# Kernel tuning notes

Hardware: AMD Instinct MI355X
Metric: run time of the kernel (lower is better)

The kernel has to match this reference:

```python
import jax, jax.numpy as jnp
import numpy as np


def _conv(x, w, b, pad):
    # x: [N,C,H,W], w: [O,C,kh,kw]
    out = jax.lax.conv_general_dilated(
        x, w, window_strides=(1, 1), padding=[(pad, pad), (pad, pad)],
        dimension_numbers=("NCHW", "OIHW", "NCHW"))
    return out + b[None, :, None, None]


def _deform_conv(x, offset, mask, w, b):
    # Modulated deformable conv (DCNv2), 3x3 kernel, stride 1, pad 1, dilation 1.
    # x: [N,C,H,W], offset: [N,18,H,W] (per-point (dy,dx) pairs), mask: [N,9,H,W]
    N, C, H, W = x.shape
    KK = 9
    off = offset.reshape(N, KK, 2, H, W)
    dy, dx = off[:, :, 0], off[:, :, 1]            # [N,9,H,W]
    k = jnp.arange(3, dtype=x.dtype) - 1.0         # kernel taps -1,0,1
    ky = jnp.repeat(k, 3)                          # row-major 3x3 order
    kx = jnp.tile(k, 3)
    py = dy + ky[None, :, None, None] + jnp.arange(H, dtype=x.dtype)[None, None, :, None]
    px = dx + kx[None, :, None, None] + jnp.arange(W, dtype=x.dtype)[None, None, None, :]
    y0 = jnp.floor(py)
    x0 = jnp.floor(px)
    wy = (py - y0)[..., None]                      # [N,9,H,W,1]
    wx = (px - x0)[..., None]
    x_t = x.transpose(0, 2, 3, 1).reshape(N, H * W, C)  # [N,HW,C]

    def gather(iy, ix):
        valid = ((iy >= 0) & (iy < H) & (ix >= 0) & (ix < W)).astype(x.dtype)
        idx = (jnp.clip(iy, 0, H - 1).astype(jnp.int32) * W
               + jnp.clip(ix, 0, W - 1).astype(jnp.int32)).reshape(N, -1)
        v = jax.vmap(lambda a, i: a[i])(x_t, idx).reshape(N, KK, H, W, C)
        return v * valid[..., None]

    v00 = gather(y0, x0)
    v01 = gather(y0, x0 + 1)
    v10 = gather(y0 + 1, x0)
    v11 = gather(y0 + 1, x0 + 1)
    samp = (v00 * (1 - wy) * (1 - wx) + v01 * (1 - wy) * wx
            + v10 * wy * (1 - wx) + v11 * wy * wx)
    samp = samp * mask[..., None]                  # modulation
    O = w.shape[0]
    out = jnp.einsum("nkhwc,ock->nohw", samp, w.reshape(O, C, KK))
    return out + b[None, :, None, None]


def _res_block(x, w1, b1, w2, b2):
    # ResidualBlock_noBN: x + conv2(relu(conv1(x)))
    return x + _conv(jax.nn.relu(_conv(x, w1, b1, 1)), w2, b2, 1)


def setup_inputs() -> dict:
    key = jax.random.key(0)
    ks = jax.random.split(key, 16)
    f = jnp.float32

    def rn(k, shape, scale):
        return jax.random.normal(k, shape, dtype=f) * scale

    N, C, H, W = 2, 64, 128, 128
    inp = {}
    inp["xd"] = rn(ks[0], (N, 2 * C, H // 2, W // 2), 1.0)
    inp["xl"] = rn(ks[1], (N, C, H, W), 1.0)
    inp["xr"] = rn(ks[2], (N, C, H, W), 1.0)
    inp["up_w"] = rn(ks[3], (C, 2 * C, 2, 2), (2 * C * 4) ** -0.5)
    inp["up_b"] = jnp.zeros((C,), f)
    inp["offl_w"] = rn(ks[4], (27, 3 * C, 3, 3), 0.01 * (3 * C * 9) ** -0.5)
    inp["offl_b"] = jnp.zeros((27,), f)
    inp["dl_w"] = rn(ks[5], (C, C, 3, 3), (C * 9) ** -0.5)
    inp["dl_b"] = jnp.zeros((C,), f)
    inp["offr_w"] = rn(ks[6], (27, 3 * C, 3, 3), 0.01 * (3 * C * 9) ** -0.5)
    inp["offr_b"] = jnp.zeros((27,), f)
    inp["dr_w"] = rn(ks[7], (C, C, 3, 3), (C * 9) ** -0.5)
    inp["dr_b"] = jnp.zeros((C,), f)
    inp["cv_w"] = rn(ks[8], (C, 3 * C, 3, 3), (3 * C * 9) ** -0.5)
    inp["cv_b"] = jnp.zeros((C,), f)
    for i, nm in enumerate(["rb1_w1", "rb1_w2", "rb2_w1", "rb2_w2"]):
        inp[nm] = rn(ks[9 + i], (C, C, 3, 3), (C * 9) ** -0.5)
    for nm in ["rb1_b1", "rb1_b2", "rb2_b1", "rb2_b2"]:
        inp[nm] = jnp.zeros((C,), f)
    return inp


def reference(xd, xl, xr, up_w, up_b, offl_w, offl_b, dl_w, dl_b,
              offr_w, offr_b, dr_w, dr_b, cv_w, cv_b,
              rb1_w1, rb1_b1, rb1_w2, rb1_b2,
              rb2_w1, rb2_b1, rb2_w2, rb2_b2):
    # UP_SAMPLE: nearest x2 upsample, then k=2 conv (pad 0 -> size 2H-1)
    xd = jnp.repeat(jnp.repeat(xd, 2, axis=2), 2, axis=3)
    xd = _conv(xd, up_w, up_b, 0)
    dY = xl.shape[2] - xd.shape[2]
    dX = xl.shape[3] - xd.shape[3]
    xd = jnp.pad(xd, ((0, 0), (0, 0), (dY // 2, dY - dY // 2), (dX // 2, dX - dX // 2)))
    # left deform branch
    ol = _conv(jnp.concatenate([xl, xr, xd], axis=1), offl_w, offl_b, 1)
    off_l = ol[:, :18]                    # cat(o1, o2)
    mask_l = jax.nn.sigmoid(ol[:, 18:])
    xl = _deform_conv(xl, off_l, mask_l, dl_w, dl_b)
    # right deform branch (uses updated xl)
    orr = _conv(jnp.concatenate([xl, xr, xd], axis=1), offr_w, offr_b, 1)
    off_r = orr[:, :18]
    mask_r = jax.nn.sigmoid(orr[:, 18:])
    xr = _deform_conv(xr, off_r, mask_r, dr_w, dr_b)
    # CONV_BLOCK: conv+relu then two residual blocks
    x = jnp.concatenate([xl, xr, xd], axis=1)
    x = jax.nn.relu(_conv(x, cv_w, cv_b, 1))
    x = _res_block(x, rb1_w1, rb1_b1, rb1_w2, rb1_b2)
    x = _res_block(x, rb2_w1, rb2_b1, rb2_w2, rb2_b2)
    return x
```

## Files before the change

kernel.cpp:

```cpp
#include <hip/hip_runtime.h>
#include <math.h>

#define HW 16384

typedef unsigned short u16;
typedef __attribute__((ext_vector_type(8))) short short8;
typedef __attribute__((ext_vector_type(16))) float f32x16;

union U16B {
  uint4 u;
  short8 v;
  u16 s[8];
};

__device__ inline u16 f2b(float f) {
  unsigned u = __float_as_uint(f);
  u += 0x7FFF + ((u >> 16) & 1);
  return (u16)(u >> 16);
}
__device__ inline float b2f(u16 h) {
  return __uint_as_float(((unsigned)h) << 16);
}

__device__ inline u16 pack_frag(const float* __restrict__ w, int Cin, int O,
                                int OT, int d) {
  int j = d & 7;
  int lane = (d >> 3) & 63;
  int rest = d >> 9;
  int ot = rest % OT; rest /= OT;
  int ks = rest & 3; rest >>= 2;
  int kx = rest % 3; rest /= 3;
  int ky = rest % 3; int s = rest / 3;
  int och = ot * 32 + (lane & 31);
  int ch = s * 64 + ks * 16 + ((lane >> 5) << 3) + j;
  if (och >= O) return 0;
  return f2b(w[((size_t)och * Cin + ch) * 9 + ky * 3 + kx]);
}

__device__ inline u16 pack_def(const float* __restrict__ w, int d) {
  int j = d & 7;
  int lane = (d >> 3) & 63;
  int g = d >> 9;
  int ot = g & 1;
  int t = g >> 1;
  int ks = t & 3;
  int k = t >> 2;
  int och = ot * 32 + (lane & 31);
  int c = ks * 16 + ((lane >> 5) << 3) + j;
  return f2b(w[((size_t)och * 64 + c) * 9 + k]);
}

__device__ inline u16 pack_up(const float* __restrict__ w, int d) {
  int j = d & 7;
  int lane = (d >> 3) & 63;
  int g = d >> 9;
  int ot = g & 1;
  int rest = g >> 1;
  int ks = rest & 7;
  int t = rest >> 3;
  int och = ot * 32 + (lane & 31);
  int ci = ks * 16 + ((lane >> 5) << 3) + j;
  return f2b(w[((size_t)och * 128 + ci) * 4 + t]);
}

__global__ __launch_bounds__(256) void setup_kernel(
    const float* __restrict__ dl_w, const float* __restrict__ dr_w,
    const float* __restrict__ up_w, const float* __restrict__ cv_w,
    const float* __restrict__ offl_w, const float* __restrict__ offr_w,
    const float* __restrict__ r1a, const float* __restrict__ r1b,
    const float* __restrict__ r2a, const float* __restrict__ r2b,
    u16* __restrict__ wup, u16* __restrict__ wdl, u16* __restrict__ wdr,
    u16* __restrict__ wcv, u16* __restrict__ wofl, u16* __restrict__ wofr,
    u16* __restrict__ wr1a, u16* __restrict__ wr1b,
    u16* __restrict__ wr2a, u16* __restrict__ wr2b,
    const float* __restrict__ xl, const float* __restrict__ xr,
    u16* __restrict__ xlh, u16* __restrict__ xrh,
    const float* __restrict__ xd, u16* __restrict__ xdh) {
  __shared__ float sT[8448];
  int tid = threadIdx.x;
  int b = blockIdx.x;
  if (b < 1856) {
    int d = b * 256 + tid;
    if (d < 32768) { wup[d] = pack_up(up_w, d); return; }
    d -= 32768;
    if (d < 36864) { wdl[d] = pack_def(dl_w, d); return; }
    d -= 36864;
    if (d < 36864) { wdr[d] = pack_def(dr_w, d); return; }
    d -= 36864;
    if (d < 110592) { wcv[d] = pack_frag(cv_w, 192, 64, 2, d); return; }
    d -= 110592;
    if (d < 55296) { wofl[d] = pack_frag(offl_w, 192, 27, 1, d); return; }
    d -= 55296;
    if (d < 55296) { wofr[d] = pack_frag(offr_w, 192, 27, 1, d); return; }
    d -= 55296;
    if (d < 36864) { wr1a[d] = pack_frag(r1a, 64, 64, 2, d); return; }
    d -= 36864;
    if (d < 36864) { wr1b[d] = pack_frag(r1b, 64, 64, 2, d); return; }
    d -= 36864;
    if (d < 36864) { wr2a[d] = pack_frag(r2a, 64, 64, 2, d); return; }
    d -= 36864;
    if (d < 36864) { wr2b[d] = pack_frag(r2b, 64, 64, 2, d); return; }
    return;
  }
  b -= 1856;
  if (b < 512) {
    int y = b & 127;
    int pid = b >> 7;
    const float* src = (pid >> 1) ? xr : xl;
    u16* dst = (pid >> 1) ? xrh : xlh;
    int n = pid & 1;
#pragma unroll
    for (int i = 0; i < 8; ++i) {
      int q = tid + i * 256;
      int ch = q >> 5, pxq = q & 31;
      float4 v = *(const float4*)(src + ((size_t)(n * 64 + ch)) * HW + y * 128 + pxq * 4);
      *(float4*)&sT[ch * 132 + pxq * 4] = v;
    }
    __syncthreads();
    int px = tid >> 1, half = tid & 1;
    u16* op = dst + (((size_t)(n * 128 + y)) * 128 + px) * 64 + half * 32;
#pragma unroll
    for (int c = 0; c < 4; ++c) {
      uint4 v;
      int ob = (half * 32 + c * 8);
      v.x = (unsigned)f2b(sT[(ob + 0) * 132 + px]) | ((unsigned)f2b(sT[(ob + 1) * 132 + px]) << 16);
      v.y = (unsigned)f2b(sT[(ob + 2) * 132 + px]) | ((unsigned)f2b(sT[(ob + 3) * 132 + px]) << 16);
      v.z = (unsigned)f2b(sT[(ob + 4) * 132 + px]) | ((unsigned)f2b(sT[(ob + 5) * 132 + px]) << 16);
      v.w = (unsigned)f2b(sT[(ob + 6) * 132 + px]) | ((unsigned)f2b(sT[(ob + 7) * 132 + px]) << 16);
      *(uint4*)(op + c * 8) = v;
    }
    return;
  }
  b -= 512;
  {
    int r = b & 63;
    int n = b >> 6;
#pragma unroll
    for (int i = 0; i < 8; ++i) {
      int q = tid + i * 256;
      int ch = q >> 4, col4 = q & 15;
      float4 v = *(const float4*)(xd + ((size_t)(n * 128 + ch) * 64 + r) * 64 + col4 * 4);
      *(float4*)&sT[ch * 66 + col4 * 4] = v;
    }
    __syncthreads();
#pragma unroll
    for (int i = 0; i < 4; ++i) {
      int q = tid + i * 256;
      int col = q >> 4, cho = q & 15;
      uint4 v;
      int cb = cho * 8;
      v.x = (unsigned)f2b(sT[(cb + 0) * 66 + col]) | ((unsigned)f2b(sT[(cb + 1) * 66 + col]) << 16);
      v.y = (unsigned)f2b(sT[(cb + 2) * 66 + col]) | ((unsigned)f2b(sT[(cb + 3) * 66 + col]) << 16);
      v.z = (unsigned)f2b(sT[(cb + 4) * 66 + col]) | ((unsigned)f2b(sT[(cb + 5) * 66 + col]) << 16);
      v.w = (unsigned)f2b(sT[(cb + 6) * 66 + col]) | ((unsigned)f2b(sT[(cb + 7) * 66 + col]) << 16);
      *(uint4*)(xdh + (((size_t)(n * 64 + r)) * 64 + col) * 128 + cb) = v;
    }
  }
}

__global__ __launch_bounds__(1024) void upconv_mf(
    const u16* __restrict__ xdh, const u16* __restrict__ wup,
    const float* __restrict__ bias, u16* __restrict__ outH) {
  __shared__ float s_red[4][3][16][64];
  const int tid = threadIdx.x;
  const int lane = tid & 63;
  const int w = tid >> 6;
  const int p2 = w >> 2;
  const int t = w & 3;
  const int y = blockIdx.x;
  const int n = blockIdx.y;
  const int px = (p2 << 5) + (lane & 31);
  const int h = lane >> 5;

  f32x16 acc0, acc1;
#pragma unroll
  for (int i = 0; i < 16; ++i) { acc0[i] = 0.f; acc1[i] = 0.f; }

  const u16* xb = xdh + ((size_t)n * 64 * 64) * 128;
  const int ty = t >> 1, tx = t & 1;
  const int row = min((y + ty) >> 1, 63);
  const int col = min((px + tx) >> 1, 63);
  const u16* src = xb + ((size_t)(row * 64 + col)) * 128;
#pragma unroll
  for (int ks = 0; ks < 8; ++ks) {
    U16B bf;
    bf.u = *(const uint4*)(src + ks * 16 + h * 8);
    const u16* wp = wup + ((size_t)((t * 8 + ks) * 2)) * 512 + lane * 8;
    U16B a0, a1;
    a0.u = *(const uint4*)wp;
    a1.u = *(const uint4*)(wp + 512);
    acc0 = __builtin_amdgcn_mfma_f32_32x32x16_bf16(a0.v, bf.v, acc0, 0, 0, 0);
    acc1 = __builtin_amdgcn_mfma_f32_32x32x16_bf16(a1.v, bf.v, acc1, 0, 0, 0);
  }

  const bool zero = (y == 127) || (px == 127);
  const size_t pixb = (((size_t)(n * 128 + y)) * 128 + px) * 64;

  if (t != 0) {
#pragma unroll
    for (int i = 0; i < 16; ++i) s_red[p2][t - 1][i][lane] = acc0[i];
  }
  __syncthreads();
  if (t == 0) {
#pragma unroll
    for (int q = 0; q < 4; ++q) {
      int oo = 8 * q + 4 * h;
      float v[4];
#pragma unroll
      for (int r = 0; r < 4; ++r) {
        int i = q * 4 + r;
        float s = acc0[i] + s_red[p2][0][i][lane] + s_red[p2][1][i][lane] +
                  s_red[p2][2][i][lane];
        v[r] = zero ? 0.f : (s + bias[oo + r]);
      }
      ushort4 hh;
      hh.x = f2b(v[0]); hh.y = f2b(v[1]); hh.z = f2b(v[2]); hh.w = f2b(v[3]);
      *(ushort4*)(outH + pixb + oo) = hh;
    }
  }
  __syncthreads();
  if (t != 0) {
#pragma unroll
    for (int i = 0; i < 16; ++i) s_red[p2][t - 1][i][lane] = acc1[i];
  }
  __syncthreads();
  if (t == 0) {
#pragma unroll
    for (int q = 0; q < 4; ++q) {
      int oo = 32 + 8 * q + 4 * h;
      float v[4];
#pragma unroll
      for (int r = 0; r < 4; ++r) {
        int i = q * 4 + r;
        float s = acc1[i] + s_red[p2][0][i][lane] + s_red[p2][1][i][lane] +
                  s_red[p2][2][i][lane];
        v[r] = zero ? 0.f : (s + bias[oo + r]);
      }
      ushort4 hh;
      hh.x = f2b(v[0]); hh.y = f2b(v[1]); hh.z = f2b(v[2]); hh.w = f2b(v[3]);
      *(ushort4*)(outH + pixb + oo) = hh;
    }
  }
}

template <int NSEG>
__global__ __launch_bounds__(1024) void mfconv_s(
    const u16* __restrict__ in0, const u16* __restrict__ in1,
    const u16* __restrict__ in2, const u16* __restrict__ wpk,
    const float* __restrict__ bias, const u16* __restrict__ resh,
    float* __restrict__ outF, u16* __restrict__ outH, int mode) {
  __shared__ __align__(16) unsigned char s_un[49920];
  u16* stg = (u16*)s_un;
  float* s_redf = (float*)s_un;

  const int tid = threadIdx.x;
  const int lane = tid & 63;
  const int w = tid >> 6;
  const int p2 = w >> 2;
  const int kq = w & 3;
  const int y = blockIdx.x;
  const int n = blockIdx.y;
  const int px = (p2 << 5) + (lane & 31);
  const int h = lane >> 5;
  const int gpx = lane >> 3;
  const int gcs = lane & 7;

  auto stg_at = [&](int e, int cg, int p) -> u16* {
    return stg + (((e * 8 + cg) * 130 + p) << 3);
  };

  f32x16 acc0, acc1;
#pragma unroll
  for (int i = 0; i < 16; ++i) { acc0[i] = 0.f; acc1[i] = 0.f; }

  for (int s = 0; s < NSEG; ++s) {
    const u16* sp = (s == 0) ? in0 : ((s == 1) ? in1 : in2);
    const u16* bn = sp + ((size_t)n * 128) * 128 * 64;
    for (int i = w; i < 48; i += 16) {
      int ky = i >> 4, g = i & 15;
      int row = y + ky - 1;
      int ppx = g * 8 + gpx;
      uint4 v = make_uint4(0, 0, 0, 0);
      if ((unsigned)row < 128u)
        v = *(const uint4*)(bn + (size_t)row * (128 * 64) + (size_t)ppx * 64 + gcs * 8);
      *(uint4*)stg_at(ky, gcs, ppx) = v;
    }
    __syncthreads();
#pragma unroll
    for (int ky = 0; ky < 3; ++ky) {
#pragma unroll
      for (int kx = 0; kx < 3; ++kx) {
        int pxc = px + kx - 1;
        bool valid = (unsigned)pxc < 128u;
        int pxcc = min(max(pxc, 0), 127);
        U16B bf;
        bf.u = *(const uint4*)stg_at(ky, kq * 2 + h, pxcc);
        if (!valid) bf.u = make_uint4(0, 0, 0, 0);
        const u16* wp = wpk +
            ((size_t)((((s * 3 + ky) * 3 + kx) * 4 + kq) * 2)) * 512 + lane * 8;
        U16B a0, a1;
        a0.u = *(const uint4*)wp;
        a1.u = *(const uint4*)(wp + 512);
        acc0 = __builtin_amdgcn_mfma_f32_32x32x16_bf16(a0.v, bf.v, acc0, 0, 0, 0);
        acc1 = __builtin_amdgcn_mfma_f32_32x32x16_bf16(a1.v, bf.v, acc1, 0, 0, 0);
      }
    }
    __syncthreads();
  }

  const size_t pixb = ((size_t)(n * 128 + y)) * 128 + px;

  if (kq != 0) {
#pragma unroll
    for (int i = 0; i < 16; ++i)
      s_redf[((p2 * 3 + (kq - 1)) * 16 + i) * 64 + lane] = acc0[i];
  }
  __syncthreads();
  if (kq == 0) {
#pragma unroll
    for (int q = 0; q < 4; ++q) {
      int oo = 8 * q + 4 * h;
      float v[4];
#pragma unroll
      for (int r = 0; r < 4; ++r) {
        int i = q * 4 + r;
        v[r] = acc0[i] + s_redf[((p2 * 3 + 0) * 16 + i) * 64 + lane] +
               s_redf[((p2 * 3 + 1) * 16 + i) * 64 + lane] +
               s_redf[((p2 * 3 + 2) * 16 + i) * 64 + lane] + bias[oo + r];
      }
      if (mode == 1) {
#pragma unroll
        for (int r = 0; r < 4; ++r) v[r] = fmaxf(v[r], 0.f);
      } else if (mode == 3) {
        ushort4 rv = *(const ushort4*)(resh + pixb * 64 + oo);
        v[0] += b2f(rv.x); v[1] += b2f(rv.y); v[2] += b2f(rv.z); v[3] += b2f(rv.w);
      }
      if (outH) {
        ushort4 hh;
        hh.x = f2b(v[0]); hh.y = f2b(v[1]); hh.z = f2b(v[2]); hh.w = f2b(v[3]);
        *(ushort4*)(outH + pixb * 64 + oo) = hh;
      } else {
#pragma unroll
        for (int r = 0; r < 4; ++r)
          outF[((size_t)(n * 64 + oo + r)) * HW + y * 128 + px] = v[r];
      }
    }
  }
  __syncthreads();
  if (kq != 0) {
#pragma unroll
    for (int i = 0; i < 16; ++i)
      s_redf[((p2 * 3 + (kq - 1)) * 16 + i) * 64 + lane] = acc1[i];
  }
  __syncthreads();
  if (kq == 0) {
#pragma unroll
    for (int q = 0; q < 4; ++q) {
      int oo = 32 + 8 * q + 4 * h;
      float v[4];
#pragma unroll
      for (int r = 0; r < 4; ++r) {
        int i = q * 4 + r;
        v[r] = acc1[i] + s_redf[((p2 * 3 + 0) * 16 + i) * 64 + lane] +
               s_redf[((p2 * 3 + 1) * 16 + i) * 64 + lane] +
               s_redf[((p2 * 3 + 2) * 16 + i) * 64 + lane] + bias[oo + r];
      }
      if (mode == 1) {
#pragma unroll
        for (int r = 0; r < 4; ++r) v[r] = fmaxf(v[r], 0.f);
      } else if (mode == 3) {
        ushort4 rv = *(const ushort4*)(resh + pixb * 64 + oo);
        v[0] += b2f(rv.x); v[1] += b2f(rv.y); v[2] += b2f(rv.z); v[3] += b2f(rv.w);
      }
      if (outH) {
        ushort4 hh;
        hh.x = f2b(v[0]); hh.y = f2b(v[1]); hh.z = f2b(v[2]); hh.w = f2b(v[3]);
        *(ushort4*)(outH + pixb * 64 + oo) = hh;
      } else {
#pragma unroll
        for (int r = 0; r < 4; ++r)
          outF[((size_t)(n * 64 + oo + r)) * HW + y * 128 + px] = v[r];
      }
    }
  }
}

__global__ __launch_bounds__(1024) void deform_fused(
    const u16* __restrict__ in0, const u16* __restrict__ in1,
    const u16* __restrict__ in2, const u16* __restrict__ woff,
    const float* __restrict__ boff, const u16* __restrict__ xh,
    const u16* __restrict__ wdef, const float* __restrict__ bdef,
    u16* __restrict__ outH) {
  __shared__ float s_off[27][128];
  __shared__ __align__(16) unsigned char s_un[49920];
  u16* stg = (u16*)s_un;
  float* s_redf = (float*)s_un;

  const int tid = threadIdx.x;
  const int lane = tid & 63;
  const int w = tid >> 6;
  const int p2 = w >> 2;
  const int kq = w & 3;
  const int y = blockIdx.x;
  const int n = blockIdx.y;
  const int px = (p2 << 5) + (lane & 31);
  const int h = lane >> 5;
  const int gpx = lane >> 3;
  const int gcs = lane & 7;

  auto stg_at = [&](int e, int cg, int p) -> u16* {
    return stg + (((e * 8 + cg) * 130 + p) << 3);
  };

  f32x16 acc;
#pragma unroll
  for (int i = 0; i < 16; ++i) acc[i] = 0.f;

  for (int s = 0; s < 3; ++s) {
    const u16* sp = (s == 0) ? in0 : ((s == 1) ? in1 : in2);
    const u16* bn = sp + ((size_t)n * 128) * 128 * 64;
    for (int i = w; i < 48; i += 16) {
      int ky = i >> 4, g = i & 15;
      int row = y + ky - 1;
      int ppx = g * 8 + gpx;
      uint4 v = make_uint4(0, 0, 0, 0);
      if ((unsigned)row < 128u)
        v = *(const uint4*)(bn + (size_t)row * (128 * 64) + (size_t)ppx * 64 + gcs * 8);
      *(uint4*)stg_at(ky, gcs, ppx) = v;
    }
    __syncthreads();
#pragma unroll
    for (int ky = 0; ky < 3; ++ky) {
#pragma unroll
      for (int kx = 0; kx < 3; ++kx) {
        int pxc = px + kx - 1;
        bool valid = (unsigned)pxc < 128u;
        int pxcc = min(max(pxc, 0), 127);
        U16B bf;
        bf.u = *(const uint4*)stg_at(ky, kq * 2 + h, pxcc);
        if (!valid) bf.u = make_uint4(0, 0, 0, 0);
        U16B a;
        a.u = *(const uint4*)(woff +
              ((size_t)(((s * 3 + ky) * 3 + kx) * 4 + kq)) * 512 + lane * 8);
        acc = __builtin_amdgcn_mfma_f32_32x32x16_bf16(a.v, bf.v, acc, 0, 0, 0);
      }
    }
    __syncthreads();
  }

  if (kq != 0) {
#pragma unroll
    for (int i = 0; i < 16; ++i) s_redf[((p2 * 3 + (kq - 1)) * 16 + i) * 64 + lane] = acc[i];
  }
  __syncthreads();
  if (kq == 0) {
#pragma unroll
    for (int q = 0; q < 4; ++q) {
#pragma unroll
      for (int r = 0; r < 4; ++r) {
        int och = 8 * q + 4 * h + r;
        if (och < 27) {
          int i = q * 4 + r;
          float v = acc[i] + s_redf[((p2 * 3 + 0) * 16 + i) * 64 + lane] +
                    s_redf[((p2 * 3 + 1) * 16 + i) * 64 + lane] +
                    s_redf[((p2 * 3 + 2) * 16 + i) * 64 + lane] + boff[och];
          if (och >= 18) v = 1.f / (1.f + expf(-v));
          s_off[och][px] = v;
        }
      }
    }
  }
  __syncthreads();

  f32x16 acc0, acc1;
#pragma unroll
  for (int i = 0; i < 16; ++i) { acc0[i] = 0.f; acc1[i] = 0.f; }

  const u16* xb = xh + ((size_t)n * HW) * 64;

  for (int tc = 0; tc < 3; ++tc) {
    for (int i = w; i < 48; i += 16) {
      int tt = i >> 4, g = i & 15;
      int t = tc * 3 + tt;
      int ppx = g * 8 + gpx;
      int ky = t / 3 - 1, kx = t % 3 - 1;
      float dy = s_off[2 * t][ppx];
      float dx = s_off[2 * t + 1][ppx];
      float m = s_off[18 + t][ppx];
      float py = dy + (float)(y + ky);
      float pxf = dx + (float)(ppx + kx);
      float fy = floorf(py), fxx = floorf(pxf);
      float wy = py - fy, wx = pxf - fxx;
      int iy0 = (int)fy, ix0 = (int)fxx;
      bool vy0 = (unsigned)iy0 < 128u, vy1 = (unsigned)(iy0 + 1) < 128u;
      bool vx0 = (unsigned)ix0 < 128u, vx1 = (unsigned)(ix0 + 1) < 128u;
      float omwy = 1.f - wy, omwx = 1.f - wx;
      float f00 = (vy0 && vx0) ? omwy * omwx * m : 0.f;
      float f01 = (vy0 && vx1) ? omwy * wx * m : 0.f;
      float f10 = (vy1 && vx0) ? wy * omwx * m : 0.f;
      float f11 = (vy1 && vx1) ? wy * wx * m : 0.f;
      int y0c = min(max(iy0, 0), 127), y1c = min(max(iy0 + 1, 0), 127);
      int x0c = min(max(ix0, 0), 127), x1c = min(max(ix0 + 1, 0), 127);
      U16B v00, v01, v10, v11;
      v00.u = *(const uint4*)(xb + ((size_t)(y0c * 128 + x0c)) * 64 + gcs * 8);
      v01.u = *(const uint4*)(xb + ((size_t)(y0c * 128 + x1c)) * 64 + gcs * 8);
      v10.u = *(const uint4*)(xb + ((size_t)(y1c * 128 + x0c)) * 64 + gcs * 8);
      v11.u = *(const uint4*)(xb + ((size_t)(y1c * 128 + x1c)) * 64 + gcs * 8);
      unsigned dw[4];
#pragma unroll
      for (int jj = 0; jj < 4; ++jj) {
        float s0 = f00 * b2f(v00.s[2 * jj]) + f01 * b2f(v01.s[2 * jj]) +
                   f10 * b2f(v10.s[2 * jj]) + f11 * b2f(v11.s[2 * jj]);
        float s1 = f00 * b2f(v00.s[2 * jj + 1]) + f01 * b2f(v01.s[2 * jj + 1]) +
                   f10 * b2f(v10.s[2 * jj + 1]) + f11 * b2f(v11.s[2 * jj + 1]);
        dw[jj] = (unsigned)f2b(s0) | ((unsigned)f2b(s1) << 16);
      }
      *(uint4*)stg_at(tt, gcs, ppx) = make_uint4(dw[0], dw[1], dw[2], dw[3]);
    }
    __syncthreads();
#pragma unroll
    for (int tt = 0; tt < 3; ++tt) {
      int t = tc * 3 + tt;
      U16B bf;
      bf.u = *(const uint4*)stg_at(tt, kq * 2 + h, px);
      const u16* wp = wdef + ((size_t)((t * 4 + kq) * 2)) * 512 + lane * 8;
      U16B a0, a1;
      a0.u = *(const uint4*)wp;
      a1.u = *(const uint4*)(wp + 512);
      acc0 = __builtin_amdgcn_mfma_f32_32x32x16_bf16(a0.v, bf.v, acc0, 0, 0, 0);
      acc1 = __builtin_amdgcn_mfma_f32_32x32x16_bf16(a1.v, bf.v, acc1, 0, 0, 0);
    }
    __syncthreads();
  }

  const size_t pixb = (((size_t)(n * 128 + y)) * 128 + px) * 64;
  if (kq != 0) {
#pragma unroll
    for (int i = 0; i < 16; ++i) s_redf[((p2 * 3 + (kq - 1)) * 16 + i) * 64 + lane] = acc0[i];
  }
  __syncthreads();
  if (kq == 0) {
#pragma unroll
    for (int q = 0; q < 4; ++q) {
      int oo = 8 * q + 4 * h;
      float v[4];
#pragma unroll
      for (int r = 0; r < 4; ++r) {
        int i = q * 4 + r;
        v[r] = acc0[i] + s_redf[((p2 * 3 + 0) * 16 + i) * 64 + lane] +
               s_redf[((p2 * 3 + 1) * 16 + i) * 64 + lane] +
               s_redf[((p2 * 3 + 2) * 16 + i) * 64 + lane] + bdef[oo + r];
      }
      ushort4 hh;
      hh.x = f2b(v[0]); hh.y = f2b(v[1]); hh.z = f2b(v[2]); hh.w = f2b(v[3]);
      *(ushort4*)(outH + pixb + oo) = hh;
    }
  }
  __syncthreads();
  if (kq != 0) {
#pragma unroll
    for (int i = 0; i < 16; ++i) s_redf[((p2 * 3 + (kq - 1)) * 16 + i) * 64 + lane] = acc1[i];
  }
  __syncthreads();
  if (kq == 0) {
#pragma unroll
    for (int q = 0; q < 4; ++q) {
      int oo = 32 + 8 * q + 4 * h;
      float v[4];
#pragma unroll
      for (int r = 0; r < 4; ++r) {
        int i = q * 4 + r;
        v[r] = acc1[i] + s_redf[((p2 * 3 + 0) * 16 + i) * 64 + lane] +
               s_redf[((p2 * 3 + 1) * 16 + i) * 64 + lane] +
               s_redf[((p2 * 3 + 2) * 16 + i) * 64 + lane] + bdef[oo + r];
      }
      ushort4 hh;
      hh.x = f2b(v[0]); hh.y = f2b(v[1]); hh.z = f2b(v[2]); hh.w = f2b(v[3]);
      *(ushort4*)(outH + pixb + oo) = hh;
    }
  }
}

extern "C" void kernel_launch(void* const* d_in, const int* in_sizes, int n_in,
                              void* d_out, int out_size, void* d_ws, size_t ws_size,
                              hipStream_t stream) {
  const float* xd = (const float*)d_in[0];
  const float* xl = (const float*)d_in[1];
  const float* xr = (const float*)d_in[2];
  const float* up_w = (const float*)d_in[3];
  const float* up_b = (const float*)d_in[4];
  const float* offl_w = (const float*)d_in[5];
  const float* offl_b = (const float*)d_in[6];
  const float* dl_w = (const float*)d_in[7];
  const float* dl_b = (const float*)d_in[8];
  const float* offr_w = (const float*)d_in[9];
  const float* offr_b = (const float*)d_in[10];
  const float* dr_w = (const float*)d_in[11];
  const float* dr_b = (const float*)d_in[12];
  const float* cv_w = (const float*)d_in[13];
  const float* cv_b = (const float*)d_in[14];
  const float* rb1_w1 = (const float*)d_in[15];
  const float* rb1_w2 = (const float*)d_in[16];
  const float* rb2_w1 = (const float*)d_in[17];
  const float* rb2_w2 = (const float*)d_in[18];
  const float* rb1_b1 = (const float*)d_in[19];
  const float* rb1_b2 = (const float*)d_in[20];
  const float* rb2_b1 = (const float*)d_in[21];
  const float* rb2_b2 = (const float*)d_in[22];

  float* ws = (float*)d_ws;
  u16* hb = (u16*)(ws + 1769472);
  u16* xlh = hb;
  u16* xrh = hb + 2097152;
  u16* xdph = hb + 4194304;
  u16* xl2h = hb + 6291456;
  u16* xr2h = hb + 8388608;
  u16* t0h = hb + 10485760;
  u16* t1h = hb + 12582912;
  u16* t2h = hb + 14680064;
  u16* t3h = hb + 16777216;
  u16* xdh = hb + 18874368;
  u16* wcv = hb + 19922944;
  u16* wofl = hb + 20033536;
  u16* wofr = hb + 20088832;
  u16* wr1a = hb + 20144128;
  u16* wr1b = hb + 20180992;
  u16* wr2a = hb + 20217856;
  u16* wr2b = hb + 20254720;
  u16* wdl = hb + 20291584;
  u16* wdr = hb + 20328448;
  u16* wup = hb + 20365312;
  float* outp = (float*)d_out;

  hipLaunchKernelGGL(setup_kernel, dim3(2496), dim3(256), 0, stream,
                     dl_w, dr_w, up_w, cv_w, offl_w, offr_w, rb1_w1, rb1_w2,
                     rb2_w1, rb2_w2, wup, wdl, wdr, wcv, wofl, wofr, wr1a,
                     wr1b, wr2a, wr2b, xl, xr, xlh, xrh, xd, xdh);
  hipLaunchKernelGGL(upconv_mf, dim3(128, 2), dim3(1024), 0, stream,
                     xdh, wup, up_b, xdph);
  hipLaunchKernelGGL(deform_fused, dim3(128, 2), dim3(1024), 0, stream,
                     xlh, xrh, xdph, wofl, offl_b, xlh, wdl, dl_b, xl2h);
  hipLaunchKernelGGL(deform_fused, dim3(128, 2), dim3(1024), 0, stream,
                     xl2h, xrh, xdph, wofr, offr_b, xrh, wdr, dr_b, xr2h);
  hipLaunchKernelGGL(mfconv_s<3>, dim3(128, 2), dim3(1024), 0, stream,
                     xl2h, xr2h, xdph, wcv, cv_b, (const u16*)nullptr,
                     (float*)nullptr, t0h, 1);
  hipLaunchKernelGGL(mfconv_s<1>, dim3(128, 2), dim3(1024), 0, stream,
                     t0h, (const u16*)nullptr, (const u16*)nullptr, wr1a,
                     rb1_b1, (const u16*)nullptr, (float*)nullptr, t1h, 1);
  hipLaunchKernelGGL(mfconv_s<1>, dim3(128, 2), dim3(1024), 0, stream,
                     t1h, (const u16*)nullptr, (const u16*)nullptr, wr1b,
                     rb1_b2, t0h, (float*)nullptr, t2h, 3);
  hipLaunchKernelGGL(mfconv_s<1>, dim3(128, 2), dim3(1024), 0, stream,
                     t2h, (const u16*)nullptr, (const u16*)nullptr, wr2a,
                     rb2_b1, (const u16*)nullptr, (float*)nullptr, t3h, 1);
  hipLaunchKernelGGL(mfconv_s<1>, dim3(128, 2), dim3(1024), 0, stream,
                     t3h, (const u16*)nullptr, (const u16*)nullptr, wr2b,
                     rb2_b2, t2h, outp, (u16*)nullptr, 3);
}
```

Before: 137.2 us.

## Fuse each residual block's two convs into one kernel with shared-memory intermediate

```diff
diff --git a/kernel.cpp b/kernel.cpp
--- a/kernel.cpp
+++ b/kernel.cpp
@@ -385,6 +385,142 @@
   }
 }
 
+__global__ __launch_bounds__(512) void rbfuse(
+    const u16* __restrict__ in, const u16* __restrict__ w1,
+    const float* __restrict__ b1, const u16* __restrict__ w2,
+    const float* __restrict__ b2, float* __restrict__ outF,
+    u16* __restrict__ outH) {
+  __shared__ __align__(16) u16 ring[3][8][128][8];
+  __shared__ __align__(16) u16 mid[3][8][128][8];
+  const int tid = threadIdx.x;
+  const int lane = tid & 63;
+  const int w = tid >> 6;
+  const int p2 = w >> 1;
+  const int ot = w & 1;
+  const int y = blockIdx.x;
+  const int n = blockIdx.y;
+  const int px = (p2 << 5) + (lane & 31);
+  const int h = lane >> 5;
+  const int gpx = lane >> 3;
+  const int gcs = lane & 7;
+  const u16* bn = in + ((size_t)n * 128) * 128 * 64;
+
+  auto stage_row = [&](int r) {
+    int sl = ((r % 3) + 3) % 3;
+    for (int i = w; i < 16; i += 8) {
+      int ppx = i * 8 + gpx;
+      uint4 v = make_uint4(0, 0, 0, 0);
+      if ((unsigned)r < 128u)
+        v = *(const uint4*)(bn + (size_t)r * (128 * 64) + (size_t)ppx * 64 + gcs * 8);
+      *(uint4*)&ring[sl][gcs][ppx][0] = v;
+    }
+  };
+
+  auto conv1_row = [&](int rr, int r) {
+    if ((unsigned)r >= 128u) {
+      ushort4 z = make_ushort4(0, 0, 0, 0);
+#pragma unroll
+      for (int q = 0; q < 4; ++q)
+        *(ushort4*)&mid[rr][ot * 4 + q][px][4 * h] = z;
+      return;
+    }
+    f32x16 acc;
+#pragma unroll
+    for (int i = 0; i < 16; ++i) acc[i] = 0.f;
+#pragma unroll
+    for (int ky = 0; ky < 3; ++ky) {
+      int sr = r - 1 + ky;
+      int sl = ((sr % 3) + 3) % 3;
+#pragma unroll
+      for (int kx = 0; kx < 3; ++kx) {
+        int pxc = px + kx - 1;
+        bool valid = (unsigned)pxc < 128u;
+        int pxcc = min(max(pxc, 0), 127);
+#pragma unroll
+        for (int kq = 0; kq < 4; ++kq) {
+          U16B bf;
+          bf.u = *(const uint4*)&ring[sl][kq * 2 + h][pxcc][0];
+          if (!valid) bf.u = make_uint4(0, 0, 0, 0);
+          U16B a;
+          a.u = *(const uint4*)(w1 +
+                ((size_t)(((ky * 3 + kx) * 4 + kq) * 2 + ot)) * 512 + lane * 8);
+          acc = __builtin_amdgcn_mfma_f32_32x32x16_bf16(a.v, bf.v, acc, 0, 0, 0);
+        }
+      }
+    }
+#pragma unroll
+    for (int q = 0; q < 4; ++q) {
+      int oo = ot * 32 + 8 * q + 4 * h;
+      ushort4 hh;
+      hh.x = f2b(fmaxf(acc[q * 4 + 0] + b1[oo + 0], 0.f));
+      hh.y = f2b(fmaxf(acc[q * 4 + 1] + b1[oo + 1], 0.f));
+      hh.z = f2b(fmaxf(acc[q * 4 + 2] + b1[oo + 2], 0.f));
+      hh.w = f2b(fmaxf(acc[q * 4 + 3] + b1[oo + 3], 0.f));
+      *(ushort4*)&mid[rr][ot * 4 + q][px][4 * h] = hh;
+    }
+  };
+
+  stage_row(y - 2);
+  stage_row(y - 1);
+  stage_row(y);
+  __syncthreads();
+  conv1_row(0, y - 1);
+  __syncthreads();
+  stage_row(y + 1);
+  __syncthreads();
+  conv1_row(1, y);
+  __syncthreads();
+  stage_row(y + 2);
+  __syncthreads();
+  conv1_row(2, y + 1);
+  __syncthreads();
+
+  f32x16 acc;
+#pragma unroll
+  for (int i = 0; i < 16; ++i) acc[i] = 0.f;
+#pragma unroll
+  for (int ky = 0; ky < 3; ++ky) {
+#pragma unroll
+    for (int kx = 0; kx < 3; ++kx) {
+      int pxc = px + kx - 1;
+      bool valid = (unsigned)pxc < 128u;
+      int pxcc = min(max(pxc, 0), 127);
+#pragma unroll
+      for (int kq = 0; kq < 4; ++kq) {
+        U16B bf;
+        bf.u = *(const uint4*)&mid[ky][kq * 2 + h][pxcc][0];
+        if (!valid) bf.u = make_uint4(0, 0, 0, 0);
+        U16B a;
+        a.u = *(const uint4*)(w2 +
+              ((size_t)(((ky * 3 + kx) * 4 + kq) * 2 + ot)) * 512 + lane * 8);
+        acc = __builtin_amdgcn_mfma_f32_32x32x16_bf16(a.v, bf.v, acc, 0, 0, 0);
+      }
+    }
+  }
+
+  const int ysl = y % 3;
+  const size_t pixb = ((size_t)(n * 128 + y)) * 128 + px;
+#pragma unroll
+  for (int q = 0; q < 4; ++q) {
+    int oo = ot * 32 + 8 * q + 4 * h;
+    ushort4 rv = *(const ushort4*)&ring[ysl][ot * 4 + q][px][4 * h];
+    float v[4];
+    v[0] = acc[q * 4 + 0] + b2[oo + 0] + b2f(rv.x);
+    v[1] = acc[q * 4 + 1] + b2[oo + 1] + b2f(rv.y);
+    v[2] = acc[q * 4 + 2] + b2[oo + 2] + b2f(rv.z);
+    v[3] = acc[q * 4 + 3] + b2[oo + 3] + b2f(rv.w);
+    if (outH) {
+      ushort4 hh;
+      hh.x = f2b(v[0]); hh.y = f2b(v[1]); hh.z = f2b(v[2]); hh.w = f2b(v[3]);
+      *(ushort4*)(outH + pixb * 64 + oo) = hh;
+    } else {
+#pragma unroll
+      for (int r = 0; r < 4; ++r)
+        outF[((size_t)(n * 64 + oo + r)) * HW + y * 128 + px] = v[r];
+    }
+  }
+}
+
 __global__ __launch_bounds__(1024) void deform_fused(
     const u16* __restrict__ in0, const u16* __restrict__ in1,
     const u16* __restrict__ in2, const u16* __restrict__ woff,
@@ -645,16 +781,8 @@
   hipLaunchKernelGGL(mfconv_s<3>, dim3(128, 2), dim3(1024), 0, stream,
                      xl2h, xr2h, xdph, wcv, cv_b, (const u16*)nullptr,
                      (float*)nullptr, t0h, 1);
-  hipLaunchKernelGGL(mfconv_s<1>, dim3(128, 2), dim3(1024), 0, stream,
-                     t0h, (const u16*)nullptr, (const u16*)nullptr, wr1a,
-                     rb1_b1, (const u16*)nullptr, (float*)nullptr, t1h, 1);
-  hipLaunchKernelGGL(mfconv_s<1>, dim3(128, 2), dim3(1024), 0, stream,
-                     t1h, (const u16*)nullptr, (const u16*)nullptr, wr1b,
-                     rb1_b2, t0h, (float*)nullptr, t2h, 3);
-  hipLaunchKernelGGL(mfconv_s<1>, dim3(128, 2), dim3(1024), 0, stream,
-                     t2h, (const u16*)nullptr, (const u16*)nullptr, wr2a,
-                     rb2_b1, (const u16*)nullptr, (float*)nullptr, t3h, 1);
-  hipLaunchKernelGGL(mfconv_s<1>, dim3(128, 2), dim3(1024), 0, stream,
-                     t3h, (const u16*)nullptr, (const u16*)nullptr, wr2b,
-                     rb2_b2, t2h, outp, (u16*)nullptr, 3);
-}
+  hipLaunchKernelGGL(rbfuse, dim3(128, 2), dim3(512), 0, stream,
+                     t0h, wr1a, rb1_b1, wr1b, rb1_b2, (float*)nullptr, t2h);
+  hipLaunchKernelGGL(rbfuse, dim3(128, 2), dim3(512), 0, stream,
+                     t2h, wr2a, rb2_b1, wr2b, rb2_b2, outp, (u16*)nullptr);
+}
```

Result: faster. 132.4 us (-3.5%).
